# Kernel optimization log

Hardware: AMD Instinct MI355X
Metric: run time of the kernel (lower is better)

The kernel has to match this reference:

```python
import jax, jax.numpy as jnp
import numpy as np

M, IN, H, OUT, B = 64, 64, 256, 1, 4096


def setup_inputs() -> dict:
    key = jax.random.key(0)
    ks = jax.random.split(key, 7)
    s1 = 1.0 / np.sqrt(IN)
    s2 = 1.0 / np.sqrt(H)
    return {
        "xs": jax.random.normal(ks[0], (M, B, IN), dtype=jnp.float32),
        "W1": jax.random.uniform(ks[1], (M, IN, H), minval=-s1, maxval=s1, dtype=jnp.float32),
        "b1": jax.random.uniform(ks[2], (M, H), minval=-s1, maxval=s1, dtype=jnp.float32),
        "W2": jax.random.uniform(ks[3], (M, H, H), minval=-s2, maxval=s2, dtype=jnp.float32),
        "b2": jax.random.uniform(ks[4], (M, H), minval=-s2, maxval=s2, dtype=jnp.float32),
        "W3": jax.random.uniform(ks[5], (M, H, OUT), minval=-s2, maxval=s2, dtype=jnp.float32),
        "b3": jax.random.uniform(ks[6], (M, OUT), minval=-s2, maxval=s2, dtype=jnp.float32),
    }


def reference(xs, W1, b1, W2, b2, W3, b3):
    # Batched over models: [M, B, in] x [M, in, h] -> [M, B, h]
    h1 = jax.nn.relu(jnp.einsum("mbi,mih->mbh", xs, W1) + b1[:, None, :])
    h2 = jax.nn.relu(jnp.einsum("mbh,mhk->mbk", h1, W2) + b2[:, None, :])
    out = jnp.einsum("mbh,mho->mbo", h2, W3) + b3[:, None, :]
    return out  # [M, B, out]
```

## Files before the change

### kernel.cpp

```cpp
#include <hip/hip_runtime.h>
#include <hip/hip_bf16.h>

#define NMODELS 64
#define BBATCH  4096
#define IN_DIM  64
#define H_DIM   256

typedef __attribute__((ext_vector_type(8))) short short8;
typedef __attribute__((ext_vector_type(4))) float floatx4;
typedef __attribute__((ext_vector_type(4))) unsigned int uint4v;
typedef __attribute__((ext_vector_type(2))) unsigned int uint2v;

__device__ __forceinline__ unsigned short f2bf(float f) {
    unsigned int u = __builtin_bit_cast(unsigned int, f);
    return (unsigned short)((u + 0x8000u) >> 16);
}
__device__ __forceinline__ unsigned int pkbf(float a, float b) {
    __hip_bfloat162 h = __float22bfloat162_rn(make_float2(a, b));
    unsigned int u;
    __builtin_memcpy(&u, &h, 4);
    return u;
}

__global__ __launch_bounds__(256) void prep_all(const float* __restrict__ W1,
                                                const float* __restrict__ W2,
                                                const float* __restrict__ xs,
                                                unsigned short* __restrict__ w1t,
                                                unsigned short* __restrict__ w2t,
                                                unsigned short* __restrict__ xsb) {
    __shared__ float lds[64][65];
    const int bid = blockIdx.x;
    const int tid = threadIdx.x;
    if (bid >= 1280) {
        size_t g = ((size_t)(bid - 1280) * 256 + tid) * 8;
        float4 v0 = *(const float4*)(xs + g);
        float4 v1 = *(const float4*)(xs + g + 4);
        uint4v u;
        u[0] = pkbf(v0.x, v0.y); u[1] = pkbf(v0.z, v0.w);
        u[2] = pkbf(v1.x, v1.y); u[3] = pkbf(v1.z, v1.w);
        *(uint4v*)(xsb + g) = u;
        return;
    }
    const float* src;
    unsigned short* dst;
    int K, N, m, kb, nb;
    if (bid < 256) {
        m = bid >> 2; kb = 0; nb = bid & 3; K = IN_DIM; N = H_DIM;
        src = W1; dst = w1t;
    } else {
        int t = bid - 256;
        m = t >> 4; kb = (t >> 2) & 3; nb = t & 3; K = H_DIM; N = H_DIM;
        src = W2; dst = w2t;
    }
    const float* s = src + ((size_t)m * K + (size_t)kb * 64) * N + nb * 64;
    const int r = tid >> 4, c4 = (tid & 15) * 4;
#pragma unroll
    for (int p = 0; p < 4; ++p) {
        int row = p * 16 + r;
        float4 v = *(const float4*)(s + (size_t)row * N + c4);
        lds[row][c4] = v.x; lds[row][c4 + 1] = v.y;
        lds[row][c4 + 2] = v.z; lds[row][c4 + 3] = v.w;
    }
    __syncthreads();
    unsigned short* dbase = dst + ((size_t)m * N + (size_t)nb * 64) * K + kb * 64;
    const int j = tid & 7;
#pragma unroll
    for (int it = 0; it < 2; ++it) {
        int n = it * 32 + (tid >> 3);
        unsigned short tmp[8];
#pragma unroll
        for (int e = 0; e < 8; ++e) tmp[e] = f2bf(lds[j * 8 + e][n]);
        *(short8*)(dbase + (size_t)n * K + j * 8) = *(const short8*)tmp;
    }
}

template <bool XB>
__global__ __launch_bounds__(256, 2) void mlp_fused(
    const float* __restrict__ xs,
    const unsigned short* __restrict__ xsb,
    const unsigned short* __restrict__ w1t,
    const float* __restrict__ b1,
    const unsigned short* __restrict__ w2t,
    const float* __restrict__ b2,
    const float* __restrict__ w3,
    const float* __restrict__ b3,
    float* __restrict__ out)
{
    __shared__ unsigned short h1s[2][64 * 256];
    __shared__ float red[2][4][64];

    const int bid   = blockIdx.x;
    const int m     = bid & 63;
    const int chunk = bid >> 6;
    const int tid = threadIdx.x;
    const int w = tid >> 6, lane = tid & 63;
    const int q = lane >> 4, c16 = lane & 15;
    const int sw = c16 & 7;
    const int colbase = w * 64 + c16 * 4;

    const unsigned short* w1p = w1t + (size_t)m * (H_DIM * IN_DIM) + colbase * IN_DIM + q * 8;
    const unsigned short* w2p = w2t + (size_t)m * (H_DIM * H_DIM) + colbase * H_DIM + q * 8;
    const float b3v = b3[m];

#pragma unroll 1
    for (int it = 0; it < 4; ++it) {
        const int tile0 = chunk * 8 + it * 2;

        floatx4 acc[2][4][4];
#pragma unroll
        for (int t = 0; t < 2; ++t)
#pragma unroll
            for (int rb = 0; rb < 4; ++rb)
#pragma unroll
                for (int nb = 0; nb < 4; ++nb)
                    acc[t][rb][nb] = (floatx4){0.f, 0.f, 0.f, 0.f};

#pragma unroll
        for (int kb = 0; kb < 2; ++kb) {
            short8 bw[4];
#pragma unroll
            for (int nb = 0; nb < 4; ++nb)
                bw[nb] = *(const short8*)(w1p + nb * IN_DIM + kb * 32);
#pragma unroll
            for (int t = 0; t < 2; ++t)
#pragma unroll
                for (int rb = 0; rb < 4; ++rb) {
                    const size_t row = (size_t)m * BBATCH + (size_t)(tile0 + t) * 64
                                       + rb * 16 + c16;
                    short8 ax;
                    if constexpr (XB) {
                        ax = *(const short8*)(xsb + row * IN_DIM + kb * 32 + q * 8);
                    } else {
                        const float* xp = xs + row * IN_DIM + kb * 32 + q * 8;
                        float4 v0 = *(const float4*)xp;
                        float4 v1 = *(const float4*)(xp + 4);
                        uint4v u;
                        u[0] = pkbf(v0.x, v0.y); u[1] = pkbf(v0.z, v0.w);
                        u[2] = pkbf(v1.x, v1.y); u[3] = pkbf(v1.z, v1.w);
                        ax = __builtin_bit_cast(short8, u);
                    }
#pragma unroll
                    for (int nb = 0; nb < 4; ++nb)
                        acc[t][rb][nb] = __builtin_amdgcn_mfma_f32_16x16x32_bf16(
                            ax, bw[nb], acc[t][rb][nb], 0, 0, 0);
                }
        }

        {
            floatx4 b1v = *(const floatx4*)(b1 + m * H_DIM + colbase);
#pragma unroll
            for (int t = 0; t < 2; ++t)
#pragma unroll
                for (int rb = 0; rb < 4; ++rb)
#pragma unroll
                    for (int r = 0; r < 4; ++r) {
                        float v0 = fmaxf(acc[t][rb][0][r] + b1v[0], 0.f);
                        float v1 = fmaxf(acc[t][rb][1][r] + b1v[1], 0.f);
                        float v2 = fmaxf(acc[t][rb][2][r] + b1v[2], 0.f);
                        float v3 = fmaxf(acc[t][rb][3][r] + b1v[3], 0.f);
                        uint2v u; u[0] = pkbf(v0, v1); u[1] = pkbf(v2, v3);
                        int row = rb * 16 + q * 4 + r;
                        int ch = (w * 8 + (c16 >> 1)) ^ (row & 7);
                        *(uint2v*)((char*)&h1s[t][0] + row * 512 + ch * 16 + (c16 & 1) * 8) = u;
                    }
        }
        __syncthreads();

#pragma unroll
        for (int t = 0; t < 2; ++t)
#pragma unroll
            for (int rb = 0; rb < 4; ++rb)
#pragma unroll
                for (int nb = 0; nb < 4; ++nb)
                    acc[t][rb][nb] = (floatx4){0.f, 0.f, 0.f, 0.f};

#pragma unroll
        for (int kb = 0; kb < 8; ++kb) {
            short8 bv[4];
#pragma unroll
            for (int nb = 0; nb < 4; ++nb)
                bv[nb] = *(const short8*)(w2p + nb * H_DIM + kb * 32);
#pragma unroll
            for (int t = 0; t < 2; ++t) {
                short8 av[4];
#pragma unroll
                for (int rb = 0; rb < 4; ++rb)
                    av[rb] = *(const short8*)((char*)&h1s[t][0] + (rb * 16 + c16) * 512
                                              + (((kb * 4 + q) ^ sw) * 16));
#pragma unroll
                for (int nb = 0; nb < 4; ++nb)
#pragma unroll
                    for (int rb = 0; rb < 4; ++rb)
                        acc[t][rb][nb] = __builtin_amdgcn_mfma_f32_16x16x32_bf16(
                            av[rb], bv[nb], acc[t][rb][nb], 0, 0, 0);
            }
        }

        floatx4 b2v = *(const floatx4*)(b2 + m * H_DIM + colbase);
        floatx4 w3v = *(const floatx4*)(w3 + m * H_DIM + colbase);
        float p[2][4][4];
#pragma unroll
        for (int t = 0; t < 2; ++t)
#pragma unroll
            for (int rb = 0; rb < 4; ++rb)
#pragma unroll
                for (int r = 0; r < 4; ++r) p[t][rb][r] = 0.f;
#pragma unroll
        for (int t = 0; t < 2; ++t)
#pragma unroll
            for (int rb = 0; rb < 4; ++rb)
#pragma unroll
                for (int nb = 0; nb < 4; ++nb)
#pragma unroll
                    for (int r = 0; r < 4; ++r) {
                        float v = fmaxf(acc[t][rb][nb][r] + b2v[nb], 0.f);
                        p[t][rb][r] += v * w3v[nb];
                    }
#pragma unroll
        for (int off = 1; off < 16; off <<= 1)
#pragma unroll
            for (int t = 0; t < 2; ++t)
#pragma unroll
                for (int rb = 0; rb < 4; ++rb)
#pragma unroll
                    for (int r = 0; r < 4; ++r)
                        p[t][rb][r] += __shfl_xor(p[t][rb][r], off);

        if (c16 == 0) {
#pragma unroll
            for (int t = 0; t < 2; ++t)
#pragma unroll
                for (int rb = 0; rb < 4; ++rb)
#pragma unroll
                    for (int r = 0; r < 4; ++r)
                        red[t][w][rb * 16 + q * 4 + r] = p[t][rb][r];
        }
        __syncthreads();
        if (tid < 128) {
            int t = tid >> 6, rr = tid & 63;
            float s = red[t][0][rr] + red[t][1][rr] + red[t][2][rr] + red[t][3][rr] + b3v;
            out[(size_t)m * BBATCH + (tile0 + t) * 64 + rr] = s;
        }
    }
}

extern "C" void kernel_launch(void* const* d_in, const int* in_sizes, int n_in,
                              void* d_out, int out_size, void* d_ws, size_t ws_size,
                              hipStream_t stream) {
    const float* xs = (const float*)d_in[0];
    const float* W1 = (const float*)d_in[1];
    const float* b1 = (const float*)d_in[2];
    const float* W2 = (const float*)d_in[3];
    const float* b2 = (const float*)d_in[4];
    const float* W3 = (const float*)d_in[5];
    const float* b3 = (const float*)d_in[6];
    float* out = (float*)d_out;

    const size_t W1T_E = (size_t)NMODELS * H_DIM * IN_DIM;
    const size_t W2T_E = (size_t)NMODELS * H_DIM * H_DIM;
    const size_t XSB_E = (size_t)NMODELS * BBATCH * IN_DIM;
    unsigned short* w1t = (unsigned short*)d_ws;
    unsigned short* w2t = w1t + W1T_E;
    unsigned short* xsb = w2t + W2T_E;
    const bool use_xb = ws_size >= (W1T_E + W2T_E + XSB_E) * sizeof(unsigned short);

    if (use_xb) {
        prep_all<<<1280 + (int)(XSB_E / (256 * 8)), 256, 0, stream>>>(W1, W2, xs, w1t, w2t, xsb);
        mlp_fused<true><<<512, 256, 0, stream>>>(xs, xsb, w1t, b1, w2t, b2, W3, b3, out);
    } else {
        prep_all<<<1280, 256, 0, stream>>>(W1, W2, xs, w1t, w2t, xsb);
        mlp_fused<false><<<512, 256, 0, stream>>>(xs, xsb, w1t, b1, w2t, b2, W3, b3, out);
    }
}
```

Measured before the change: 214.8 us.

## Switch to 32x32x16 MFMA with transposed operands and one tile pair per block

Replaces the 16x16x32 MFMA tiling with 32x32x16 MFMAs, computing the transposed product so the weights are the A operand and the batch rows are the B operand. The h1 shared-memory layout and swizzle are reworked to match. The per-block loop over four tile pairs is removed and the grid grows from 512 to 2048 blocks with model-major block indexing. The intent is fewer MFMA instructions, less cross-lane shuffle reduction and more parallelism, at the cost of reloading weights in every block.

```diff
diff --git a/kernel.cpp b/kernel.cpp
--- a/kernel.cpp
+++ b/kernel.cpp
@@ -6,10 +6,11 @@
 #define IN_DIM  64
 #define H_DIM   256
 
-typedef __attribute__((ext_vector_type(8))) short short8;
-typedef __attribute__((ext_vector_type(4))) float floatx4;
-typedef __attribute__((ext_vector_type(4))) unsigned int uint4v;
-typedef __attribute__((ext_vector_type(2))) unsigned int uint2v;
+typedef __attribute__((ext_vector_type(8)))  short short8;
+typedef __attribute__((ext_vector_type(4)))  float floatx4;
+typedef __attribute__((ext_vector_type(16))) float floatx16;
+typedef __attribute__((ext_vector_type(4)))  unsigned int uint4v;
+typedef __attribute__((ext_vector_type(2)))  unsigned int uint2v;
 
 __device__ __forceinline__ unsigned short f2bf(float f) {
     unsigned int u = __builtin_bit_cast(unsigned int, f);
@@ -90,157 +91,171 @@
     __shared__ float red[2][4][64];
 
     const int bid   = blockIdx.x;
-    const int m     = bid & 63;
-    const int chunk = bid >> 6;
+    const int m     = bid >> 5;
+    const int tile0 = (bid & 31) * 2;
     const int tid = threadIdx.x;
     const int w = tid >> 6, lane = tid & 63;
-    const int q = lane >> 4, c16 = lane & 15;
-    const int sw = c16 & 7;
-    const int colbase = w * 64 + c16 * 4;
-
-    const unsigned short* w1p = w1t + (size_t)m * (H_DIM * IN_DIM) + colbase * IN_DIM + q * 8;
-    const unsigned short* w2p = w2t + (size_t)m * (H_DIM * H_DIM) + colbase * H_DIM + q * 8;
+    const int ln = lane & 31, l5 = lane >> 5;
+
+    const unsigned short* w1m = w1t + (size_t)m * (H_DIM * IN_DIM);
+    const unsigned short* w2m = w2t + (size_t)m * (H_DIM * H_DIM);
     const float b3v = b3[m];
 
-#pragma unroll 1
-    for (int it = 0; it < 4; ++it) {
-        const int tile0 = chunk * 8 + it * 2;
-
-        floatx4 acc[2][4][4];
-#pragma unroll
-        for (int t = 0; t < 2; ++t)
-#pragma unroll
-            for (int rb = 0; rb < 4; ++rb)
-#pragma unroll
-                for (int nb = 0; nb < 4; ++nb)
-                    acc[t][rb][nb] = (floatx4){0.f, 0.f, 0.f, 0.f};
-
-#pragma unroll
-        for (int kb = 0; kb < 2; ++kb) {
-            short8 bw[4];
-#pragma unroll
-            for (int nb = 0; nb < 4; ++nb)
-                bw[nb] = *(const short8*)(w1p + nb * IN_DIM + kb * 32);
+    floatx16 acc[2][2][2];
+#pragma unroll
+    for (int t = 0; t < 2; ++t)
+#pragma unroll
+        for (int mb = 0; mb < 2; ++mb)
+#pragma unroll
+            for (int nb = 0; nb < 2; ++nb)
+#pragma unroll
+                for (int i = 0; i < 16; ++i) acc[t][mb][nb][i] = 0.f;
+
+#pragma unroll
+    for (int ks = 0; ks < 4; ++ks) {
+        short8 a1[2];
+#pragma unroll
+        for (int mb = 0; mb < 2; ++mb)
+            a1[mb] = *(const short8*)(w1m + (size_t)(w * 64 + mb * 32 + ln) * IN_DIM
+                                      + ks * 16 + l5 * 8);
+        short8 xb[2][2];
+#pragma unroll
+        for (int t = 0; t < 2; ++t)
+#pragma unroll
+            for (int nb = 0; nb < 2; ++nb) {
+                const size_t row = (size_t)m * BBATCH + (size_t)(tile0 + t) * 64
+                                   + nb * 32 + ln;
+                if constexpr (XB) {
+                    xb[t][nb] = *(const short8*)(xsb + row * IN_DIM + ks * 16 + l5 * 8);
+                } else {
+                    const float* xp = xs + row * IN_DIM + ks * 16 + l5 * 8;
+                    float4 v0 = *(const float4*)xp;
+                    float4 v1 = *(const float4*)(xp + 4);
+                    uint4v u;
+                    u[0] = pkbf(v0.x, v0.y); u[1] = pkbf(v0.z, v0.w);
+                    u[2] = pkbf(v1.x, v1.y); u[3] = pkbf(v1.z, v1.w);
+                    xb[t][nb] = __builtin_bit_cast(short8, u);
+                }
+            }
+#pragma unroll
+        for (int t = 0; t < 2; ++t)
+#pragma unroll
+            for (int mb = 0; mb < 2; ++mb)
+#pragma unroll
+                for (int nb = 0; nb < 2; ++nb)
+                    acc[t][mb][nb] = __builtin_amdgcn_mfma_f32_32x32x16_bf16(
+                        a1[mb], xb[t][nb], acc[t][mb][nb], 0, 0, 0);
+    }
+
+    {
+        floatx4 b1v[2][4];
+#pragma unroll
+        for (int mb = 0; mb < 2; ++mb)
+#pragma unroll
+            for (int rg = 0; rg < 4; ++rg)
+                b1v[mb][rg] = *(const floatx4*)(b1 + m * H_DIM + w * 64 + mb * 32
+                                                + rg * 8 + l5 * 4);
+#pragma unroll
+        for (int t = 0; t < 2; ++t)
+#pragma unroll
+            for (int mb = 0; mb < 2; ++mb)
+#pragma unroll
+                for (int nb = 0; nb < 2; ++nb) {
+                    const int row = nb * 32 + ln;
+                    char* base = (char*)&h1s[t][0] + row * 512;
+                    const int swz = row & 14;
+#pragma unroll
+                    for (int rg = 0; rg < 4; ++rg) {
+                        float v0 = fmaxf(acc[t][mb][nb][rg * 4 + 0] + b1v[mb][rg][0], 0.f);
+                        float v1 = fmaxf(acc[t][mb][nb][rg * 4 + 1] + b1v[mb][rg][1], 0.f);
+                        float v2 = fmaxf(acc[t][mb][nb][rg * 4 + 2] + b1v[mb][rg][2], 0.f);
+                        float v3 = fmaxf(acc[t][mb][nb][rg * 4 + 3] + b1v[mb][rg][3], 0.f);
+                        uint2v u; u[0] = pkbf(v0, v1); u[1] = pkbf(v2, v3);
+                        const int chunk = (w * 16 + mb * 8 + rg * 2 + l5) ^ swz;
+                        *(uint2v*)(base + chunk * 8) = u;
+                    }
+                }
+    }
+    __syncthreads();
+
+#pragma unroll
+    for (int t = 0; t < 2; ++t)
+#pragma unroll
+        for (int mb = 0; mb < 2; ++mb)
+#pragma unroll
+            for (int nb = 0; nb < 2; ++nb)
+#pragma unroll
+                for (int i = 0; i < 16; ++i) acc[t][mb][nb][i] = 0.f;
+
+#pragma unroll
+    for (int ks = 0; ks < 16; ++ks) {
+        short8 a2[2];
+#pragma unroll
+        for (int mb = 0; mb < 2; ++mb)
+            a2[mb] = *(const short8*)(w2m + (size_t)(w * 64 + mb * 32 + ln) * H_DIM
+                                      + ks * 16 + l5 * 8);
+        short8 hb[2][2];
+#pragma unroll
+        for (int t = 0; t < 2; ++t)
+#pragma unroll
+            for (int nb = 0; nb < 2; ++nb) {
+                const int row = nb * 32 + ln;
+                const int chunk = (ks * 4 + l5 * 2) ^ (row & 14);
+                hb[t][nb] = *(const short8*)((char*)&h1s[t][0] + row * 512 + chunk * 8);
+            }
+#pragma unroll
+        for (int t = 0; t < 2; ++t)
+#pragma unroll
+            for (int mb = 0; mb < 2; ++mb)
+#pragma unroll
+                for (int nb = 0; nb < 2; ++nb)
+                    acc[t][mb][nb] = __builtin_amdgcn_mfma_f32_32x32x16_bf16(
+                        a2[mb], hb[t][nb], acc[t][mb][nb], 0, 0, 0);
+    }
+
+    {
+        floatx4 b2v[2][4], w3v[2][4];
+#pragma unroll
+        for (int mb = 0; mb < 2; ++mb)
+#pragma unroll
+            for (int rg = 0; rg < 4; ++rg) {
+                b2v[mb][rg] = *(const floatx4*)(b2 + m * H_DIM + w * 64 + mb * 32
+                                                + rg * 8 + l5 * 4);
+                w3v[mb][rg] = *(const floatx4*)(w3 + m * H_DIM + w * 64 + mb * 32
+                                                + rg * 8 + l5 * 4);
+            }
+        float p[2][2] = {{0.f, 0.f}, {0.f, 0.f}};
+#pragma unroll
+        for (int t = 0; t < 2; ++t)
+#pragma unroll
+            for (int mb = 0; mb < 2; ++mb)
+#pragma unroll
+                for (int nb = 0; nb < 2; ++nb)
+#pragma unroll
+                    for (int rg = 0; rg < 4; ++rg)
+#pragma unroll
+                        for (int i = 0; i < 4; ++i) {
+                            float v = fmaxf(acc[t][mb][nb][rg * 4 + i] + b2v[mb][rg][i], 0.f);
+                            p[t][nb] += v * w3v[mb][rg][i];
+                        }
+#pragma unroll
+        for (int t = 0; t < 2; ++t)
+#pragma unroll
+            for (int nb = 0; nb < 2; ++nb)
+                p[t][nb] += __shfl_xor(p[t][nb], 32);
+        if (l5 == 0) {
 #pragma unroll
             for (int t = 0; t < 2; ++t)
 #pragma unroll
-                for (int rb = 0; rb < 4; ++rb) {
-                    const size_t row = (size_t)m * BBATCH + (size_t)(tile0 + t) * 64
-                                       + rb * 16 + c16;
-                    short8 ax;
-                    if constexpr (XB) {
-                        ax = *(const short8*)(xsb + row * IN_DIM + kb * 32 + q * 8);
-                    } else {
-                        const float* xp = xs + row * IN_DIM + kb * 32 + q * 8;
-                        float4 v0 = *(const float4*)xp;
-                        float4 v1 = *(const float4*)(xp + 4);
-                        uint4v u;
-                        u[0] = pkbf(v0.x, v0.y); u[1] = pkbf(v0.z, v0.w);
-                        u[2] = pkbf(v1.x, v1.y); u[3] = pkbf(v1.z, v1.w);
-                        ax = __builtin_bit_cast(short8, u);
-                    }
-#pragma unroll
-                    for (int nb = 0; nb < 4; ++nb)
-                        acc[t][rb][nb] = __builtin_amdgcn_mfma_f32_16x16x32_bf16(
-                            ax, bw[nb], acc[t][rb][nb], 0, 0, 0);
-                }
+                for (int nb = 0; nb < 2; ++nb)
+                    red[t][w][nb * 32 + ln] = p[t][nb];
         }
-
-        {
-            floatx4 b1v = *(const floatx4*)(b1 + m * H_DIM + colbase);
-#pragma unroll
-            for (int t = 0; t < 2; ++t)
-#pragma unroll
-                for (int rb = 0; rb < 4; ++rb)
-#pragma unroll
-                    for (int r = 0; r < 4; ++r) {
-                        float v0 = fmaxf(acc[t][rb][0][r] + b1v[0], 0.f);
-                        float v1 = fmaxf(acc[t][rb][1][r] + b1v[1], 0.f);
-                        float v2 = fmaxf(acc[t][rb][2][r] + b1v[2], 0.f);
-                        float v3 = fmaxf(acc[t][rb][3][r] + b1v[3], 0.f);
-                        uint2v u; u[0] = pkbf(v0, v1); u[1] = pkbf(v2, v3);
-                        int row = rb * 16 + q * 4 + r;
-                        int ch = (w * 8 + (c16 >> 1)) ^ (row & 7);
-                        *(uint2v*)((char*)&h1s[t][0] + row * 512 + ch * 16 + (c16 & 1) * 8) = u;
-                    }
-        }
-        __syncthreads();
-
-#pragma unroll
-        for (int t = 0; t < 2; ++t)
-#pragma unroll
-            for (int rb = 0; rb < 4; ++rb)
-#pragma unroll
-                for (int nb = 0; nb < 4; ++nb)
-                    acc[t][rb][nb] = (floatx4){0.f, 0.f, 0.f, 0.f};
-
-#pragma unroll
-        for (int kb = 0; kb < 8; ++kb) {
-            short8 bv[4];
-#pragma unroll
-            for (int nb = 0; nb < 4; ++nb)
-                bv[nb] = *(const short8*)(w2p + nb * H_DIM + kb * 32);
-#pragma unroll
-            for (int t = 0; t < 2; ++t) {
-                short8 av[4];
-#pragma unroll
-                for (int rb = 0; rb < 4; ++rb)
-                    av[rb] = *(const short8*)((char*)&h1s[t][0] + (rb * 16 + c16) * 512
-                                              + (((kb * 4 + q) ^ sw) * 16));
-#pragma unroll
-                for (int nb = 0; nb < 4; ++nb)
-#pragma unroll
-                    for (int rb = 0; rb < 4; ++rb)
-                        acc[t][rb][nb] = __builtin_amdgcn_mfma_f32_16x16x32_bf16(
-                            av[rb], bv[nb], acc[t][rb][nb], 0, 0, 0);
-            }
-        }
-
-        floatx4 b2v = *(const floatx4*)(b2 + m * H_DIM + colbase);
-        floatx4 w3v = *(const floatx4*)(w3 + m * H_DIM + colbase);
-        float p[2][4][4];
-#pragma unroll
-        for (int t = 0; t < 2; ++t)
-#pragma unroll
-            for (int rb = 0; rb < 4; ++rb)
-#pragma unroll
-                for (int r = 0; r < 4; ++r) p[t][rb][r] = 0.f;
-#pragma unroll
-        for (int t = 0; t < 2; ++t)
-#pragma unroll
-            for (int rb = 0; rb < 4; ++rb)
-#pragma unroll
-                for (int nb = 0; nb < 4; ++nb)
-#pragma unroll
-                    for (int r = 0; r < 4; ++r) {
-                        float v = fmaxf(acc[t][rb][nb][r] + b2v[nb], 0.f);
-                        p[t][rb][r] += v * w3v[nb];
-                    }
-#pragma unroll
-        for (int off = 1; off < 16; off <<= 1)
-#pragma unroll
-            for (int t = 0; t < 2; ++t)
-#pragma unroll
-                for (int rb = 0; rb < 4; ++rb)
-#pragma unroll
-                    for (int r = 0; r < 4; ++r)
-                        p[t][rb][r] += __shfl_xor(p[t][rb][r], off);
-
-        if (c16 == 0) {
-#pragma unroll
-            for (int t = 0; t < 2; ++t)
-#pragma unroll
-                for (int rb = 0; rb < 4; ++rb)
-#pragma unroll
-                    for (int r = 0; r < 4; ++r)
-                        red[t][w][rb * 16 + q * 4 + r] = p[t][rb][r];
-        }
-        __syncthreads();
-        if (tid < 128) {
-            int t = tid >> 6, rr = tid & 63;
-            float s = red[t][0][rr] + red[t][1][rr] + red[t][2][rr] + red[t][3][rr] + b3v;
-            out[(size_t)m * BBATCH + (tile0 + t) * 64 + rr] = s;
-        }
+    }
+    __syncthreads();
+    if (tid < 128) {
+        int t = tid >> 6, rr = tid & 63;
+        float s = red[t][0][rr] + red[t][1][rr] + red[t][2][rr] + red[t][3][rr] + b3v;
+        out[(size_t)m * BBATCH + (tile0 + t) * 64 + rr] = s;
     }
 }
 
@@ -266,9 +281,11 @@
 
     if (use_xb) {
         prep_all<<<1280 + (int)(XSB_E / (256 * 8)), 256, 0, stream>>>(W1, W2, xs, w1t, w2t, xsb);
-        mlp_fused<true><<<512, 256, 0, stream>>>(xs, xsb, w1t, b1, w2t, b2, W3, b3, out);
+        mlp_fused<true><<<NMODELS * (BBATCH / 128), 256, 0, stream>>>(
+            xs, xsb, w1t, b1, w2t, b2, W3, b3, out);
     } else {
         prep_all<<<1280, 256, 0, stream>>>(W1, W2, xs, w1t, w2t, xsb);
-        mlp_fused<false><<<512, 256, 0, stream>>>(xs, xsb, w1t, b1, w2t, b2, W3, b3, out);
-    }
-}
+        mlp_fused<false><<<NMODELS * (BBATCH / 128), 256, 0, stream>>>(
+            xs, xsb, w1t, b1, w2t, b2, W3, b3, out);
+    }
+}
```

Result: faster. 207.0 us (-3.6%).
